# Kernel optimization log

Hardware: AMD Instinct MI355X
Metric: run time of the kernel (lower is better)

## Reference

```python
import jax, jax.numpy as jnp
import numpy as np

B, T, C, H = 4, 2048, 1024, 16
DH = C // H  # 64


def setup_inputs() -> dict:
    key = jax.random.key(0)
    ks = jax.random.split(key, 9)
    s = 1.0 / np.sqrt(C)
    return {
        "x": jax.random.normal(ks[0], (B, T, C), dtype=jnp.float32),
        "Wq": jax.random.normal(ks[1], (C, C), dtype=jnp.float32) * s,
        "bq": jax.random.normal(ks[2], (C,), dtype=jnp.float32) * 0.01,
        "Wk": jax.random.normal(ks[3], (C, C), dtype=jnp.float32) * s,
        "bk": jax.random.normal(ks[4], (C,), dtype=jnp.float32) * 0.01,
        "Wv": jax.random.normal(ks[5], (C, C), dtype=jnp.float32) * s,
        "bv": jax.random.normal(ks[6], (C,), dtype=jnp.float32) * 0.01,
        "Wo": jax.random.normal(ks[7], (C, C), dtype=jnp.float32) * s,
        "bo": jax.random.normal(ks[8], (C,), dtype=jnp.float32) * 0.01,
    }


def reference(x, Wq, bq, Wk, bk, Wv, bv, Wo, bo):
    b, t, c = x.shape
    # q,k,v: [B, H, T, DH]
    def heads(W, bias):
        return (x @ W.T + bias).reshape(b, t, H, DH).transpose(0, 2, 1, 3)
    q = heads(Wq, bq)
    k = heads(Wk, bk)
    v = heads(Wv, bv)
    scale = 1.0 / np.sqrt(DH)
    att = jnp.einsum('bhqd,bhkd->bhqk', q, k) * scale  # [B,H,T,T]
    # causal mask (is_causal=True)
    causal = jnp.tril(jnp.ones((t, t), dtype=bool))
    att = jnp.where(causal[None, None], att, -jnp.inf)
    att = jax.nn.softmax(att, axis=-1)
    y = jnp.einsum('bhqk,bhkd->bhqd', att, v)  # [B,H,T,DH]
    y = y.transpose(0, 2, 1, 3).reshape(b, t, c)
    return y @ Wo.T + bo
```

## Files before the change

### kernel.cpp

```cpp
#include <hip/hip_runtime.h>


typedef _Float16 fp16x8 __attribute__((ext_vector_type(8)));
typedef _Float16 fp16x2 __attribute__((ext_vector_type(2)));
typedef float f32x4 __attribute__((ext_vector_type(4)));

#define LOG2E 1.44269504088896f
#define M_FIX 10.0f

__device__ __forceinline__ void async_ld16(const _Float16* g, _Float16* l) {
  __builtin_amdgcn_global_load_lds(
      (const __attribute__((address_space(1))) void*)g,
      (__attribute__((address_space(3))) void*)l, 16, 0, 0);
}

__global__ __launch_bounds__(256) void cast_all(
    const float* __restrict__ x, const float* __restrict__ wq, const float* __restrict__ wk,
    const float* __restrict__ wv, const float* __restrict__ wo,
    _Float16* __restrict__ xh, _Float16* __restrict__ wcat, _Float16* __restrict__ woh) {
  const int bid = blockIdx.x;
  const float* s;
  _Float16* d;
  int off;
  if (bid < 4096) {
    s = x; d = xh; off = bid * 2048;
  } else {
    const int t = bid - 4096;
    const int wi = t >> 9;
    off = (t & 511) * 2048;
    s = (wi == 0) ? wq : (wi == 1) ? wk : (wi == 2) ? wv : wo;
    d = (wi < 3) ? (wcat + wi * 1048576) : woh;
  }
  const int i = off + threadIdx.x * 8;
  float4 a = *(const float4*)(s + i);
  float4 b = *(const float4*)(s + i + 4);
  fp16x8 h;
  h[0] = (_Float16)a.x; h[1] = (_Float16)a.y; h[2] = (_Float16)a.z; h[3] = (_Float16)a.w;
  h[4] = (_Float16)b.x; h[5] = (_Float16)b.y; h[6] = (_Float16)b.z; h[7] = (_Float16)b.w;
  *(fp16x8*)(d + i) = h;
}

__global__ __launch_bounds__(256) void gemm_qkv(
    const _Float16* __restrict__ A, const _Float16* __restrict__ W,
    const float* __restrict__ bq, const float* __restrict__ bk, const float* __restrict__ bv,
    _Float16* __restrict__ qo, _Float16* __restrict__ ko, _Float16* __restrict__ vo) {
  __shared__ __align__(16) _Float16 smem[16384];
  _Float16* As = smem;
  _Float16* Bs = smem + 4096;
  const int tid = threadIdx.x;
  const int m0 = blockIdx.x * 128;
  const int n0 = blockIdx.y * 128;
  const int w = tid >> 6, lane = tid & 63;
  const int lr = lane & 15, quad = lane >> 4;
  const int wm = (w & 1) * 64, wn = (w >> 1) * 64;

  f32x4 acc[4][4];
#pragma unroll
  for (int i = 0; i < 4; ++i)
#pragma unroll
    for (int j = 0; j < 4; ++j) acc[i][j] = (f32x4){0.f, 0.f, 0.f, 0.f};

  const int sr1 = tid >> 2, sc = (tid & 3) * 8, sr2 = sr1 + 64;
  const _Float16* Ag1 = A + (size_t)(m0 + sr1) * 1024 + sc;
  const _Float16* Ag2 = A + (size_t)(m0 + sr2) * 1024 + sc;
  const _Float16* Bg1 = W + (size_t)(n0 + sr1) * 1024 + sc;
  const _Float16* Bg2 = W + (size_t)(n0 + sr2) * 1024 + sc;
  _Float16* Ad1 = &As[sr1 * 32 + sc];
  _Float16* Ad2 = &As[sr2 * 32 + sc];
  _Float16* Bd1 = &Bs[sr1 * 32 + sc];
  _Float16* Bd2 = &Bs[sr2 * 32 + sc];

  for (int kt = 0; kt < 32; ++kt) {
    const int kk = kt * 32;
    __syncthreads();
    async_ld16(Ag1 + kk, Ad1);
    async_ld16(Ag2 + kk, Ad2);
    async_ld16(Bg1 + kk, Bd1);
    async_ld16(Bg2 + kk, Bd2);
    __syncthreads();
    fp16x8 af[4], bf[4];
#pragma unroll
    for (int i = 0; i < 4; ++i) {
      af[i] = *(const fp16x8*)&As[(wm + i * 16 + lr) * 32 + quad * 8];
      bf[i] = *(const fp16x8*)&Bs[(wn + i * 16 + lr) * 32 + quad * 8];
    }
#pragma unroll
    for (int i = 0; i < 4; ++i)
#pragma unroll
      for (int j = 0; j < 4; ++j)
        acc[i][j] = __builtin_amdgcn_mfma_f32_16x16x32_f16(af[i], bf[j], acc[i][j], 0, 0, 0);
  }

  const int wsel = n0 >> 10;
  const float* bias = (wsel == 0) ? bq : (wsel == 1) ? bk : bv;
  _Float16* dst = (wsel == 0) ? qo : (wsel == 1) ? ko : vo;
  float bv4[4];
#pragma unroll
  for (int j = 0; j < 4; ++j) bv4[j] = bias[(n0 + wn + j * 16 + lr) & 1023];

  __syncthreads();
  _Float16* Tr = smem + w * 4096;
#pragma unroll
  for (int j = 0; j < 4; ++j) {
    const int C = j * 16 + lr, ch = C >> 3, cin = C & 7;
#pragma unroll
    for (int i = 0; i < 4; ++i)
#pragma unroll
      for (int r = 0; r < 4; ++r) {
        const int R = i * 16 + quad * 4 + r;
        Tr[R * 64 + ((ch ^ (R & 7)) << 3) + cin] = (_Float16)(acc[i][j][r] + bv4[j]);
      }
  }
  const int r8 = lane >> 3, c8 = lane & 7;
  const int h = ((n0 + wn) & 1023) >> 6;
#pragma unroll
  for (int ch = 0; ch < 8; ++ch) {
    const int Rl = ch * 8 + r8;
    fp16x8 vv = *(const fp16x8*)&Tr[Rl * 64 + ((c8 ^ r8) << 3)];
    const int m = m0 + wm + Rl;
    const int b = m >> 11, t = m & 2047;
    *(fp16x8*)&dst[((size_t)(b * 16 + h) * 2048 + t) * 64 + c8 * 8] = vv;
  }
}

__global__ __launch_bounds__(256) void gemm_out(
    const _Float16* __restrict__ A, const _Float16* __restrict__ W,
    const float* __restrict__ bo, float* __restrict__ out) {
  __shared__ __align__(16) _Float16 smem[16384];
  _Float16* As = smem;
  _Float16* Bs = smem + 4096;
  const int tid = threadIdx.x;
  const int m0 = blockIdx.x * 128;
  const int n0 = blockIdx.y * 128;
  const int w = tid >> 6, lane = tid & 63;
  const int lr = lane & 15, quad = lane >> 4;
  const int wm = (w & 1) * 64, wn = (w >> 1) * 64;

  f32x4 acc[4][4];
#pragma unroll
  for (int i = 0; i < 4; ++i)
#pragma unroll
    for (int j = 0; j < 4; ++j) acc[i][j] = (f32x4){0.f, 0.f, 0.f, 0.f};

  const int sr1 = tid >> 2, sc = (tid & 3) * 8, sr2 = sr1 + 64;
  const _Float16* Ag1 = A + (size_t)(m0 + sr1) * 1024 + sc;
  const _Float16* Ag2 = A + (size_t)(m0 + sr2) * 1024 + sc;
  const _Float16* Bg1 = W + (size_t)(n0 + sr1) * 1024 + sc;
  const _Float16* Bg2 = W + (size_t)(n0 + sr2) * 1024 + sc;
  _Float16* Ad1 = &As[sr1 * 32 + sc];
  _Float16* Ad2 = &As[sr2 * 32 + sc];
  _Float16* Bd1 = &Bs[sr1 * 32 + sc];
  _Float16* Bd2 = &Bs[sr2 * 32 + sc];

  for (int kt = 0; kt < 32; ++kt) {
    const int kk = kt * 32;
    __syncthreads();
    async_ld16(Ag1 + kk, Ad1);
    async_ld16(Ag2 + kk, Ad2);
    async_ld16(Bg1 + kk, Bd1);
    async_ld16(Bg2 + kk, Bd2);
    __syncthreads();
    fp16x8 af[4], bf[4];
#pragma unroll
    for (int i = 0; i < 4; ++i) {
      af[i] = *(const fp16x8*)&As[(wm + i * 16 + lr) * 32 + quad * 8];
      bf[i] = *(const fp16x8*)&Bs[(wn + i * 16 + lr) * 32 + quad * 8];
    }
#pragma unroll
    for (int i = 0; i < 4; ++i)
#pragma unroll
      for (int j = 0; j < 4; ++j)
        acc[i][j] = __builtin_amdgcn_mfma_f32_16x16x32_f16(af[i], bf[j], acc[i][j], 0, 0, 0);
  }

  float bv4[4];
#pragma unroll
  for (int j = 0; j < 4; ++j) bv4[j] = bo[n0 + wn + j * 16 + lr];

  __syncthreads();
  float* Trf = (float*)smem + w * 2048;
  const int r16 = lane >> 4, c16 = lane & 15;
#pragma unroll
  for (int t2 = 0; t2 < 2; ++t2) {
#pragma unroll
    for (int i2 = 0; i2 < 2; ++i2) {
      const int i = t2 * 2 + i2;
#pragma unroll
      for (int j = 0; j < 4; ++j) {
        const int C = j * 16 + lr, ch = C >> 2, cin = C & 3;
#pragma unroll
        for (int r = 0; r < 4; ++r) {
          const int R = i2 * 16 + quad * 4 + r;
          Trf[R * 64 + ((ch ^ (R & 15)) << 2) + cin] = acc[i][j][r] + bv4[j];
        }
      }
    }
#pragma unroll
    for (int ch4 = 0; ch4 < 8; ++ch4) {
      const int Rl = ch4 * 4 + r16;
      float4 vv = *(const float4*)&Trf[Rl * 64 + ((c16 ^ (Rl & 15)) << 2)];
      *(float4*)&out[(size_t)(m0 + wm + t2 * 32 + Rl) * 1024 + n0 + wn + c16 * 4] = vv;
    }
  }
}

__global__ __launch_bounds__(256) void attn(
    const _Float16* __restrict__ q, const _Float16* __restrict__ k,
    const _Float16* __restrict__ v, _Float16* __restrict__ y) {
  __shared__ __align__(16) _Float16 Ks[64 * 64];
  __shared__ __align__(16) _Float16 Vt[64 * 64];
  __shared__ __align__(16) _Float16 Ps[4 * 32 * 64];
  const int tid = threadIdx.x;
  const int w = tid >> 6, lane = tid & 63;
  const int lr = lane & 15, quad = lane >> 4;
  const int lr7 = lr & 7;
  const int bx = blockIdx.x;
  const int bh = blockIdx.y;
  const int b = bh >> 4, h = bh & 15;
  const size_t base = (size_t)bh * 2048 * 64;
  _Float16* Pw = &Ps[w * 32 * 64];

  const int mlo = bx * 64 + w * 16;
  const int mhi = (31 - bx) * 64 + w * 16;

  const int kr = tid >> 2, kcb = (tid & 3) * 16, kch = (tid & 3) * 2;
  const int vkp = (tid & 31) * 2, vdb8 = (tid >> 5) * 8;
  const int vch = (tid & 31) >> 2, vin = vkp & 7;

  const _Float16 qs = (_Float16)(0.125f * LOG2E);
  fp16x8 qlo[2], qhi[2];
#pragma unroll
  for (int c = 0; c < 2; ++c) {
    fp16x8 t0 = *(const fp16x8*)(q + base + (size_t)(mlo + lr) * 64 + c * 32 + quad * 8);
    fp16x8 t1 = *(const fp16x8*)(q + base + (size_t)(mhi + lr) * 64 + c * 32 + quad * 8);
#pragma unroll
    for (int i = 0; i < 8; ++i) { t0[i] = t0[i] * qs; t1[i] = t1[i] * qs; }
    qlo[c] = t0; qhi[c] = t1;
  }

  fp16x8 onesv;
#pragma unroll
  for (int i = 0; i < 8; ++i) onesv[i] = (_Float16)1.0f;

  f32x4 olo[4], ohi[4], l5lo, l5hi;
#pragma unroll
  for (int dt = 0; dt < 4; ++dt) {
    olo[dt] = (f32x4){0.f, 0.f, 0.f, 0.f};
    ohi[dt] = (f32x4){0.f, 0.f, 0.f, 0.f};
  }
  l5lo = (f32x4){0.f, 0.f, 0.f, 0.f};
  l5hi = (f32x4){0.f, 0.f, 0.f, 0.f};

  const int ntiles = 32 - bx;
  fp16x8 ka, kb, va, vb;
  {
    const _Float16* kg = k + base + (size_t)kr * 64 + kcb;
    const _Float16* vg = v + base + (size_t)vkp * 64 + vdb8;
    ka = *(const fp16x8*)kg; kb = *(const fp16x8*)(kg + 8);
    va = *(const fp16x8*)vg; vb = *(const fp16x8*)(vg + 64);
  }

  const f32x4 cinit = (f32x4){-M_FIX, -M_FIX, -M_FIX, -M_FIX};

  for (int kt = 0; kt < ntiles; ++kt) {
    __syncthreads();
    *(fp16x8*)&Ks[kr * 64 + ((kch ^ (kr & 7)) << 3)] = ka;
    *(fp16x8*)&Ks[kr * 64 + (((kch + 1) ^ (kr & 7)) << 3)] = kb;
#pragma unroll
    for (int i = 0; i < 8; ++i) {
      fp16x2 p; p[0] = va[i]; p[1] = vb[i];
      *(fp16x2*)&Vt[(vdb8 + i) * 64 + ((vch ^ i) << 3) + vin] = p;
    }
    __syncthreads();
    if (kt + 1 < ntiles) {
      const _Float16* kg = k + base + (size_t)((kt + 1) * 64 + kr) * 64 + kcb;
      const _Float16* vg = v + base + (size_t)((kt + 1) * 64 + vkp) * 64 + vdb8;
      ka = *(const fp16x8*)kg; kb = *(const fp16x8*)(kg + 8);
      va = *(const fp16x8*)vg; vb = *(const fp16x8*)(vg + 64);
    }

    const bool lo_on = (kt <= bx);
    f32x4 shi[4], slo[4];
#pragma unroll
    for (int kct = 0; kct < 4; ++kct) { shi[kct] = cinit; slo[kct] = cinit; }
#pragma unroll
    for (int kct = 0; kct < 4; ++kct) {
      fp16x8 kf0 = *(const fp16x8*)&Ks[(kct * 16 + lr) * 64 + ((quad ^ lr7) << 3)];
      fp16x8 kf1 = *(const fp16x8*)&Ks[(kct * 16 + lr) * 64 + (((4 + quad) ^ lr7) << 3)];
      shi[kct] = __builtin_amdgcn_mfma_f32_16x16x32_f16(qhi[0], kf0, shi[kct], 0, 0, 0);
      shi[kct] = __builtin_amdgcn_mfma_f32_16x16x32_f16(qhi[1], kf1, shi[kct], 0, 0, 0);
      if (lo_on) {
        slo[kct] = __builtin_amdgcn_mfma_f32_16x16x32_f16(qlo[0], kf0, slo[kct], 0, 0, 0);
        slo[kct] = __builtin_amdgcn_mfma_f32_16x16x32_f16(qlo[1], kf1, slo[kct], 0, 0, 0);
      }
    }

    const int pr7 = (quad * 4) & 7;
    {
      const bool dmask = (kt == ntiles - 1);
      const int qrow0 = mhi + quad * 4;
#pragma unroll
      for (int kct = 0; kct < 4; ++kct) {
        const int kc = kt * 64 + kct * 16 + lr;
        const int ch = 2 * kct + (lr >> 3);
#pragma unroll
        for (int r = 0; r < 4; ++r) {
          float p = __builtin_amdgcn_exp2f(shi[kct][r]);
          if (dmask && kc > qrow0 + r) p = 0.f;
          Pw[(16 + quad * 4 + r) * 64 + ((ch ^ ((pr7 + r) & 7)) << 3) + lr7] = (_Float16)p;
        }
      }
    }
    if (lo_on) {
      const bool dmask = (kt == bx);
      const int qrow0 = mlo + quad * 4;
#pragma unroll
      for (int kct = 0; kct < 4; ++kct) {
        const int kc = kt * 64 + kct * 16 + lr;
        const int ch = 2 * kct + (lr >> 3);
#pragma unroll
        for (int r = 0; r < 4; ++r) {
          float p = __builtin_amdgcn_exp2f(slo[kct][r]);
          if (dmask && kc > qrow0 + r) p = 0.f;
          Pw[(quad * 4 + r) * 64 + ((ch ^ ((pr7 + r) & 7)) << 3) + lr7] = (_Float16)p;
        }
      }
    }

#pragma unroll
    for (int c = 0; c < 2; ++c) {
      const int sch = ((c * 4 + quad) ^ lr7) << 3;
      fp16x8 pf_hi = *(const fp16x8*)&Pw[(16 + lr) * 64 + sch];
      fp16x8 pf_lo;
      if (lo_on) pf_lo = *(const fp16x8*)&Pw[lr * 64 + sch];
      l5hi = __builtin_amdgcn_mfma_f32_16x16x32_f16(pf_hi, onesv, l5hi, 0, 0, 0);
      if (lo_on) l5lo = __builtin_amdgcn_mfma_f32_16x16x32_f16(pf_lo, onesv, l5lo, 0, 0, 0);
#pragma unroll
      for (int dt = 0; dt < 4; ++dt) {
        fp16x8 vf = *(const fp16x8*)&Vt[(dt * 16 + lr) * 64 + sch];
        ohi[dt] = __builtin_amdgcn_mfma_f32_16x16x32_f16(pf_hi, vf, ohi[dt], 0, 0, 0);
        if (lo_on)
          olo[dt] = __builtin_amdgcn_mfma_f32_16x16x32_f16(pf_lo, vf, olo[dt], 0, 0, 0);
      }
    }
  }

#pragma unroll
  for (int r = 0; r < 4; ++r) {
    const float ilo = 1.f / l5lo[r];
    const float ihi = 1.f / l5hi[r];
    const int tlo = mlo + quad * 4 + r;
    const int thi = mhi + quad * 4 + r;
    _Float16* yplo = y + ((size_t)(b * 2048 + tlo)) * 1024 + h * 64;
    _Float16* yphi = y + ((size_t)(b * 2048 + thi)) * 1024 + h * 64;
#pragma unroll
    for (int dt = 0; dt < 4; ++dt) {
      yplo[dt * 16 + lr] = (_Float16)(olo[dt][r] * ilo);
      yphi[dt * 16 + lr] = (_Float16)(ohi[dt][r] * ihi);
    }
  }
}

extern "C" void kernel_launch(void* const* d_in, const int* in_sizes, int n_in,
                              void* d_out, int out_size, void* d_ws, size_t ws_size,
                              hipStream_t stream) {
  const float* x  = (const float*)d_in[0];
  const float* Wq = (const float*)d_in[1];
  const float* bq = (const float*)d_in[2];
  const float* Wk = (const float*)d_in[3];
  const float* bk = (const float*)d_in[4];
  const float* Wv = (const float*)d_in[5];
  const float* bv = (const float*)d_in[6];
  const float* Wo = (const float*)d_in[7];
  const float* bo = (const float*)d_in[8];

  _Float16* ws   = (_Float16*)d_ws;
  _Float16* xh   = ws;
  _Float16* Wcat = xh + 8388608;
  _Float16* Woh  = Wcat + 3145728;
  _Float16* qh   = Woh + 1048576;
  _Float16* kh   = qh + 8388608;
  _Float16* vh   = kh + 8388608;
  _Float16* yh   = xh;

  cast_all<<<6144, 256, 0, stream>>>(x, Wq, Wk, Wv, Wo, xh, Wcat, Woh);
  gemm_qkv<<<dim3(64, 24), 256, 0, stream>>>(xh, Wcat, bq, bk, bv, qh, kh, vh);
  attn<<<dim3(16, 64), 256, 0, stream>>>(qh, kh, vh, yh);
  gemm_out<<<dim3(64, 8), 256, 0, stream>>>(yh, Woh, bo, (float*)d_out);
}
```

Measured before the change: 295.1 us.

## Keep attention probabilities in registers via transposed S=K·Qᵀ MFMA layout

Computes the score tile transposed (K as the A operand, Q as B) so each lane holds four consecutive key probabilities for one query. These feed directly as the B operand of 16x16x16 MFMAs against V read from LDS, which removes the P round-trip through shared memory and the ones-vector MFMA used for row sums. Row sums are now accumulated in registers and reduced across lanes with shuffles, and output stores become 4-wide vectors. In exchange, the PV step uses the smaller-K 16x16x16 MFMA, which means more instructions and more V fragment loads from LDS.

```diff
diff --git a/kernel.cpp b/kernel.cpp
--- a/kernel.cpp
+++ b/kernel.cpp
@@ -2,6 +2,7 @@
 
 
 typedef _Float16 fp16x8 __attribute__((ext_vector_type(8)));
+typedef _Float16 fp16x4 __attribute__((ext_vector_type(4)));
 typedef _Float16 fp16x2 __attribute__((ext_vector_type(2)));
 typedef float f32x4 __attribute__((ext_vector_type(4)));
 
@@ -209,7 +210,6 @@
     const _Float16* __restrict__ v, _Float16* __restrict__ y) {
   __shared__ __align__(16) _Float16 Ks[64 * 64];
   __shared__ __align__(16) _Float16 Vt[64 * 64];
-  __shared__ __align__(16) _Float16 Ps[4 * 32 * 64];
   const int tid = threadIdx.x;
   const int w = tid >> 6, lane = tid & 63;
   const int lr = lane & 15, quad = lane >> 4;
@@ -218,7 +218,6 @@
   const int bh = blockIdx.y;
   const int b = bh >> 4, h = bh & 15;
   const size_t base = (size_t)bh * 2048 * 64;
-  _Float16* Pw = &Ps[w * 32 * 64];
 
   const int mlo = bx * 64 + w * 16;
   const int mhi = (31 - bx) * 64 + w * 16;
@@ -238,18 +237,18 @@
     qlo[c] = t0; qhi[c] = t1;
   }
 
-  fp16x8 onesv;
-#pragma unroll
-  for (int i = 0; i < 8; ++i) onesv[i] = (_Float16)1.0f;
-
-  f32x4 olo[4], ohi[4], l5lo, l5hi;
+  int voff[4];
+#pragma unroll
+  for (int kct = 0; kct < 4; ++kct)
+    voff[kct] = (((kct * 2 + (quad >> 1)) ^ lr7) << 3) + (quad & 1) * 4;
+
+  f32x4 olo[4], ohi[4];
 #pragma unroll
   for (int dt = 0; dt < 4; ++dt) {
     olo[dt] = (f32x4){0.f, 0.f, 0.f, 0.f};
     ohi[dt] = (f32x4){0.f, 0.f, 0.f, 0.f};
   }
-  l5lo = (f32x4){0.f, 0.f, 0.f, 0.f};
-  l5hi = (f32x4){0.f, 0.f, 0.f, 0.f};
+  float lplo = 0.f, lphi = 0.f;
 
   const int ntiles = 32 - bx;
   fp16x8 ka, kb, va, vb;
@@ -282,82 +281,77 @@
     const bool lo_on = (kt <= bx);
     f32x4 shi[4], slo[4];
 #pragma unroll
-    for (int kct = 0; kct < 4; ++kct) { shi[kct] = cinit; slo[kct] = cinit; }
-#pragma unroll
     for (int kct = 0; kct < 4; ++kct) {
       fp16x8 kf0 = *(const fp16x8*)&Ks[(kct * 16 + lr) * 64 + ((quad ^ lr7) << 3)];
       fp16x8 kf1 = *(const fp16x8*)&Ks[(kct * 16 + lr) * 64 + (((4 + quad) ^ lr7) << 3)];
-      shi[kct] = __builtin_amdgcn_mfma_f32_16x16x32_f16(qhi[0], kf0, shi[kct], 0, 0, 0);
-      shi[kct] = __builtin_amdgcn_mfma_f32_16x16x32_f16(qhi[1], kf1, shi[kct], 0, 0, 0);
+      shi[kct] = __builtin_amdgcn_mfma_f32_16x16x32_f16(kf0, qhi[0], cinit, 0, 0, 0);
+      shi[kct] = __builtin_amdgcn_mfma_f32_16x16x32_f16(kf1, qhi[1], shi[kct], 0, 0, 0);
       if (lo_on) {
-        slo[kct] = __builtin_amdgcn_mfma_f32_16x16x32_f16(qlo[0], kf0, slo[kct], 0, 0, 0);
-        slo[kct] = __builtin_amdgcn_mfma_f32_16x16x32_f16(qlo[1], kf1, slo[kct], 0, 0, 0);
-      }
-    }
-
-    const int pr7 = (quad * 4) & 7;
+        slo[kct] = __builtin_amdgcn_mfma_f32_16x16x32_f16(kf0, qlo[0], cinit, 0, 0, 0);
+        slo[kct] = __builtin_amdgcn_mfma_f32_16x16x32_f16(kf1, qlo[1], slo[kct], 0, 0, 0);
+      }
+    }
+
     {
       const bool dmask = (kt == ntiles - 1);
-      const int qrow0 = mhi + quad * 4;
+      const int qrow = mhi + lr;
 #pragma unroll
       for (int kct = 0; kct < 4; ++kct) {
-        const int kc = kt * 64 + kct * 16 + lr;
-        const int ch = 2 * kct + (lr >> 3);
+        const int kc0 = kt * 64 + kct * 16 + quad * 4;
+        fp16x4 pf;
 #pragma unroll
         for (int r = 0; r < 4; ++r) {
           float p = __builtin_amdgcn_exp2f(shi[kct][r]);
-          if (dmask && kc > qrow0 + r) p = 0.f;
-          Pw[(16 + quad * 4 + r) * 64 + ((ch ^ ((pr7 + r) & 7)) << 3) + lr7] = (_Float16)p;
+          if (dmask && (kc0 + r) > qrow) p = 0.f;
+          lphi += p;
+          pf[r] = (_Float16)p;
+        }
+#pragma unroll
+        for (int dt = 0; dt < 4; ++dt) {
+          fp16x4 af = *(const fp16x4*)&Vt[(dt * 16 + lr) * 64 + voff[kct]];
+          ohi[dt] = __builtin_amdgcn_mfma_f32_16x16x16f16(af, pf, ohi[dt], 0, 0, 0);
         }
       }
     }
     if (lo_on) {
       const bool dmask = (kt == bx);
-      const int qrow0 = mlo + quad * 4;
+      const int qrow = mlo + lr;
 #pragma unroll
       for (int kct = 0; kct < 4; ++kct) {
-        const int kc = kt * 64 + kct * 16 + lr;
-        const int ch = 2 * kct + (lr >> 3);
+        const int kc0 = kt * 64 + kct * 16 + quad * 4;
+        fp16x4 pf;
 #pragma unroll
         for (int r = 0; r < 4; ++r) {
           float p = __builtin_amdgcn_exp2f(slo[kct][r]);
-          if (dmask && kc > qrow0 + r) p = 0.f;
-          Pw[(quad * 4 + r) * 64 + ((ch ^ ((pr7 + r) & 7)) << 3) + lr7] = (_Float16)p;
-        }
-      }
-    }
-
-#pragma unroll
-    for (int c = 0; c < 2; ++c) {
-      const int sch = ((c * 4 + quad) ^ lr7) << 3;
-      fp16x8 pf_hi = *(const fp16x8*)&Pw[(16 + lr) * 64 + sch];
-      fp16x8 pf_lo;
-      if (lo_on) pf_lo = *(const fp16x8*)&Pw[lr * 64 + sch];
-      l5hi = __builtin_amdgcn_mfma_f32_16x16x32_f16(pf_hi, onesv, l5hi, 0, 0, 0);
-      if (lo_on) l5lo = __builtin_amdgcn_mfma_f32_16x16x32_f16(pf_lo, onesv, l5lo, 0, 0, 0);
-#pragma unroll
-      for (int dt = 0; dt < 4; ++dt) {
-        fp16x8 vf = *(const fp16x8*)&Vt[(dt * 16 + lr) * 64 + sch];
-        ohi[dt] = __builtin_amdgcn_mfma_f32_16x16x32_f16(pf_hi, vf, ohi[dt], 0, 0, 0);
-        if (lo_on)
-          olo[dt] = __builtin_amdgcn_mfma_f32_16x16x32_f16(pf_lo, vf, olo[dt], 0, 0, 0);
-      }
-    }
-  }
-
-#pragma unroll
-  for (int r = 0; r < 4; ++r) {
-    const float ilo = 1.f / l5lo[r];
-    const float ihi = 1.f / l5hi[r];
-    const int tlo = mlo + quad * 4 + r;
-    const int thi = mhi + quad * 4 + r;
-    _Float16* yplo = y + ((size_t)(b * 2048 + tlo)) * 1024 + h * 64;
-    _Float16* yphi = y + ((size_t)(b * 2048 + thi)) * 1024 + h * 64;
-#pragma unroll
-    for (int dt = 0; dt < 4; ++dt) {
-      yplo[dt * 16 + lr] = (_Float16)(olo[dt][r] * ilo);
-      yphi[dt * 16 + lr] = (_Float16)(ohi[dt][r] * ihi);
-    }
+          if (dmask && (kc0 + r) > qrow) p = 0.f;
+          lplo += p;
+          pf[r] = (_Float16)p;
+        }
+#pragma unroll
+        for (int dt = 0; dt < 4; ++dt) {
+          fp16x4 af = *(const fp16x4*)&Vt[(dt * 16 + lr) * 64 + voff[kct]];
+          olo[dt] = __builtin_amdgcn_mfma_f32_16x16x16f16(af, pf, olo[dt], 0, 0, 0);
+        }
+      }
+    }
+  }
+
+  lplo += __shfl_xor(lplo, 16); lplo += __shfl_xor(lplo, 32);
+  lphi += __shfl_xor(lphi, 16); lphi += __shfl_xor(lphi, 32);
+  const float ilo = 1.f / lplo, ihi = 1.f / lphi;
+
+  _Float16* yplo = y + ((size_t)(b * 2048 + mlo + lr)) * 1024 + h * 64;
+  _Float16* yphi = y + ((size_t)(b * 2048 + mhi + lr)) * 1024 + h * 64;
+#pragma unroll
+  for (int dt = 0; dt < 4; ++dt) {
+    fp16x4 slo4, shi4;
+#pragma unroll
+    for (int r = 0; r < 4; ++r) {
+      slo4[r] = (_Float16)(olo[dt][r] * ilo);
+      shi4[r] = (_Float16)(ohi[dt][r] * ihi);
+    }
+    *(fp16x4*)&yplo[dt * 16 + quad * 4] = slo4;
+    *(fp16x4*)&yphi[dt * 16 + quad * 4] = shi4;
   }
 }
 
```

After: 275.5 us. 1.07x faster.
